# Performance work log

Measured on AMD Instinct MI355X. Metric: run time of the kernel, lower is better.

The kernel has to match this reference:

```python
import jax, jax.numpy as jnp
import numpy as np

N = 50000      # total nodes in batched graph
E = 800000     # total edges (avg degree 16)
B = 512        # number of graphs in batch
F_IN = 74      # input node feature size
H = 64         # hidden size per layer
OUT = 64       # output_feats
EPS = 1e-5     # BatchNorm eps


def setup_inputs() -> dict:
    key = jax.random.key(0)
    ks = jax.random.split(key, 32)
    d = {}
    d['feats'] = jax.random.normal(ks[0], (N, F_IN), dtype=jnp.float32)
    d['src'] = jax.random.randint(ks[1], (E,), 0, N)
    d['dst'] = jax.random.randint(ks[2], (E,), 0, N)
    d['graph_ids'] = jnp.sort(jax.random.randint(ks[3], (N,), 0, B))
    dims = [F_IN, H, H, H]
    i = 4
    for l in range(3):
        din, dout = dims[l], dims[l + 1]
        d[f'W{l}'] = jax.random.normal(ks[i], (din, dout), jnp.float32) / np.sqrt(din).astype(np.float32); i += 1
        d[f'b{l}'] = jnp.zeros((dout,), jnp.float32)
        d[f'rW{l}'] = jax.random.normal(ks[i], (din, dout), jnp.float32) / np.sqrt(din).astype(np.float32); i += 1
        d[f'rb{l}'] = jnp.zeros((dout,), jnp.float32)
        d[f'g{l}'] = jnp.ones((dout,), jnp.float32)    # BN gamma
        d[f'be{l}'] = jnp.zeros((dout,), jnp.float32)  # BN beta
    d['aw_W'] = jax.random.normal(ks[i], (H, 1), jnp.float32) / np.sqrt(H).astype(np.float32); i += 1
    d['aw_b'] = jnp.zeros((1,), jnp.float32)
    d['out_W'] = jax.random.normal(ks[i], (2 * H, OUT), jnp.float32) / np.sqrt(2 * H).astype(np.float32); i += 1
    d['out_b'] = jnp.zeros((OUT,), jnp.float32)
    return d


def _gcn_layer(x, src, dst, W, b, rW, rb, g, be):
    # GraphConv, norm='none': out = sum-aggregate(X W) + b, then relu
    xw = x @ W                                                    # [N, dout]
    agg = jax.ops.segment_sum(xw[src], dst, num_segments=N) + b   # gather/scatter over edges
    h = jax.nn.relu(agg)
    # residual: relu(Linear(x))
    h = h + jax.nn.relu(x @ rW + rb)
    # dropout p=0 -> identity
    # BatchNorm1d (training-mode batch statistics, biased variance)
    mean = jnp.mean(h, axis=0)
    var = jnp.var(h, axis=0)
    return (h - mean) * jax.lax.rsqrt(var + EPS) * g + be


def reference(feats, src, dst, graph_ids,
              W0, b0, rW0, rb0, g0, be0,
              W1, b1, rW1, rb1, g1, be1,
              W2, b2, rW2, rb2, g2, be2,
              aw_W, aw_b, out_W, out_b):
    h = feats
    h = _gcn_layer(h, src, dst, W0, b0, rW0, rb0, g0, be0)
    h = _gcn_layer(h, src, dst, W1, b1, rW1, rb1, g1, be1)
    h = _gcn_layer(h, src, dst, W2, b2, rW2, rb2, g2, be2)
    # WeightedSumAndMax readout
    w = jax.nn.sigmoid(h @ aw_W + aw_b)                               # [N, 1]
    h_sum = jax.ops.segment_sum(h * w, graph_ids, num_segments=B)     # [B, H]
    h_max = jax.ops.segment_max(h, graph_ids, num_segments=B)         # [B, H]
    h_max = jnp.where(jnp.isfinite(h_max), h_max, 0.0)                # empty graphs -> 0 (dgl max_nodes)
    h_g = jnp.concatenate([h_sum, h_max], axis=1)                     # [B, 2H]
    return h_g @ out_W + out_b                                        # [B, OUT]
```

## Files before the change

kernel.cpp:

```cpp
#include <hip/hip_runtime.h>
#include <hip/hip_bf16.h>
#include <math.h>

#define NN 50000
#define NE 800000
#define NB 512
#define FIN 74
#define HD 64
#define BN_EPS 1e-5f

#define CHUNK 32
#define ELLW 32
#define NBLK ((NN + CHUNK - 1) / CHUNK)
#define NBUCK2 NBLK
#define EB2 128
#define EPB (NE / EB2)
#define OCAP 512


__global__ void init_kernel(float* __restrict__ stats012,
                            unsigned long long* __restrict__ xw_zrow,
                            const float* __restrict__ W0, const float* __restrict__ rW0,
                            float2* __restrict__ Wpk0) {
    int i = blockIdx.x * 256 + threadIdx.x;
    if (i < 384) stats012[i] = 0.f;
    if (i < 16) xw_zrow[i] = 0ull;
    if (i < FIN * HD) Wpk0[i] = make_float2(W0[i], rW0[i]);
}

__global__ __launch_bounds__(256) void hist2_kernel(const int* __restrict__ dst,
                                                    int* __restrict__ H) {
    __shared__ int lh[NBUCK2];
    int b = blockIdx.x, tid = threadIdx.x;
    for (int i = tid; i < NBUCK2; i += 256) lh[i] = 0;
    __syncthreads();
    int e0 = b * EPB;
    for (int i = tid; i < EPB; i += 256) atomicAdd(&lh[dst[e0 + i] >> 5], 1);
    __syncthreads();
    for (int i = tid; i < NBUCK2; i += 256) H[b * NBUCK2 + i] = lh[i];
}

__global__ __launch_bounds__(128) void scanA2_kernel(int* __restrict__ H, int* __restrict__ T) {
    __shared__ int l[128];
    int k = blockIdx.x, tid = threadIdx.x;
    int v = H[tid * NBUCK2 + k];
    l[tid] = v;
    __syncthreads();
    for (int off = 1; off < 128; off <<= 1) {
        int t = (tid >= off) ? l[tid - off] : 0;
        __syncthreads();
        l[tid] += t;
        __syncthreads();
    }
    H[tid * NBUCK2 + k] = l[tid] - v;
    if (tid == 127) T[k] = l[127];
}

__global__ __launch_bounds__(256) void scanB2_kernel(const int* __restrict__ T,
                                                     int* __restrict__ bbase) {
    __shared__ int l[256];
    __shared__ int carry;
    int tid = threadIdx.x;
    if (tid == 0) carry = 0;
    __syncthreads();
    for (int c0 = 0; c0 < NBUCK2; c0 += 256) {
        int v = (c0 + tid < NBUCK2) ? T[c0 + tid] : 0;
        l[tid] = v;
        __syncthreads();
        for (int off = 1; off < 256; off <<= 1) {
            int t = (tid >= off) ? l[tid - off] : 0;
            __syncthreads();
            l[tid] += t;
            __syncthreads();
        }
        if (c0 + tid < NBUCK2) bbase[c0 + tid] = l[tid] - v + carry;
        __syncthreads();
        if (tid == 0) carry += l[255];
        __syncthreads();
    }
    if (tid == 0) bbase[NBUCK2] = carry;
}

__global__ __launch_bounds__(256) void addC_kernel(int* __restrict__ H,
                                                   const int* __restrict__ bbase) {
    int b = blockIdx.x;
    for (int k = threadIdx.x; k < NBUCK2; k += 256) H[b * NBUCK2 + k] += bbase[k];
}

__global__ __launch_bounds__(256) void scatter2_kernel(const int* __restrict__ src,
                                                       const int* __restrict__ dst,
                                                       const int* __restrict__ H,
                                                       unsigned* __restrict__ pairs) {
    __shared__ int cur[NBUCK2];
    int b = blockIdx.x, tid = threadIdx.x;
    for (int i = tid; i < NBUCK2; i += 256) cur[i] = H[b * NBUCK2 + i];
    __syncthreads();
    int e0 = b * EPB;
    for (int i = tid; i < EPB; i += 256) {
        int d = dst[e0 + i];
        int s = src[e0 + i];
        int pos = atomicAdd(&cur[d >> 5], 1);
        pairs[pos] = (unsigned)s | ((unsigned)(d & 31) << 17);
    }
}


template <int K>
__global__ __launch_bounds__(256) void gemm_dual_kernel(
    const float* __restrict__ x, const float2* __restrict__ Wpk,
    const float* __restrict__ rb, __hip_bfloat16* __restrict__ xw,
    __hip_bfloat16* __restrict__ res, int n) {
    __shared__ float2 sW[K * HD];
    __shared__ float srb[64];
    for (int i = threadIdx.x; i < K * HD; i += 256) sW[i] = Wpk[i];
    if (threadIdx.x < 64) srb[threadIdx.x] = rb[threadIdx.x];
    __syncthreads();
    int wl = threadIdx.x >> 6, lane = threadIdx.x & 63;
    for (int r0 = (blockIdx.x * 4 + wl) * 8; r0 < n; r0 += gridDim.x * 32) {
        float a1[8], a2[8];
#pragma unroll
        for (int r = 0; r < 8; ++r) { a1[r] = 0.f; a2[r] = 0.f; }
#pragma unroll
        for (int c0 = 0; c0 < K; c0 += 64) {
            const int cl = (K - c0 < 64) ? (K - c0) : 64;
            float xv[8];
#pragma unroll
            for (int r = 0; r < 8; ++r) {
                int row = r0 + r;
                xv[r] = (lane < cl && row < n) ? x[(size_t)row * K + c0 + lane] : 0.f;
            }
            for (int j = 0; j < cl; ++j) {
                float2 w = sW[(c0 + j) * HD + lane];
#pragma unroll
                for (int r = 0; r < 8; ++r) {
                    float xb = __uint_as_float(
                        __builtin_amdgcn_readlane(__float_as_uint(xv[r]), j));
                    a1[r] = fmaf(xb, w.x, a1[r]);
                    a2[r] = fmaf(xb, w.y, a2[r]);
                }
            }
        }
#pragma unroll
        for (int r = 0; r < 8; ++r) {
            int row = r0 + r;
            if (row < n) {
                xw[(size_t)row * HD + lane] = __float2bfloat16(a1[r]);
                res[(size_t)row * HD + lane] = __float2bfloat16(fmaxf(a2[r] + srb[lane], 0.f));
            }
        }
    }
}

__global__ void fold_kernel(const float* __restrict__ stats, const float* __restrict__ g,
                            const float* __restrict__ be, const float* __restrict__ W,
                            const float* __restrict__ rW, const float* __restrict__ rb,
                            float2* __restrict__ Wpk, float* __restrict__ shiftW,
                            float* __restrict__ rbp) {
    __shared__ float sc[64], sh[64];
    int t = threadIdx.x;
    if (t < 64) {
        float mean = stats[t] / (float)NN;
        float var = stats[64 + t] / (float)NN - mean * mean;
        float scale = g[t] * rsqrtf(var + BN_EPS);
        sc[t] = scale;
        sh[t] = be[t] - mean * scale;
    }
    __syncthreads();
    for (int i = t; i < 64 * 64; i += 256) {
        int k = i >> 6;
        Wpk[i] = make_float2(sc[k] * W[i], sc[k] * rW[i]);
    }
    if (t < 64) {
        float sw = 0.f, srw = 0.f;
        for (int k = 0; k < 64; ++k) {
            sw = fmaf(sh[k], W[k * 64 + t], sw);
            srw = fmaf(sh[k], rW[k * 64 + t], srw);
        }
        shiftW[t] = sw;
        rbp[t] = rb[t] + srw;
    }
}

__device__ __forceinline__ float bf_lo(unsigned int p) { return __uint_as_float(p << 16); }
__device__ __forceinline__ float bf_hi(unsigned int p) { return __uint_as_float(p & 0xffff0000u); }

#define GATHER16(BASE)                                             \
    {                                                              \
        unsigned long long d[16];                                  \
        _Pragma("unroll") for (int j = 0; j < 16; ++j) {           \
            int idx = sIdx[rloc][(BASE) + j];                      \
            unsigned off = (unsigned)idx * 16u + (unsigned)c8;     \
            d[j] = XWu[off];                                       \
        }                                                          \
        _Pragma("unroll") for (int j = 0; j < 16; ++j) {           \
            unsigned lo = (unsigned)d[j], hi = (unsigned)(d[j] >> 32); \
            a0 += bf_lo(lo); a1 += bf_hi(lo);                      \
            a2 += bf_lo(hi); a3 += bf_hi(hi);                      \
        }                                                          \
    }

__global__ __launch_bounds__(256, 4) void fused_agg_kernel(
    const __hip_bfloat16* __restrict__ xw, const __hip_bfloat16* __restrict__ res,
    const float* __restrict__ b, const float* __restrict__ shiftW,
    const int* __restrict__ bbase, const unsigned* __restrict__ pairs,
    float* __restrict__ hout, float* __restrict__ stats, int n) {
    __shared__ int sIdx[CHUNK][ELLW + 1];
    __shared__ int sLen[CHUNK];
    __shared__ unsigned oflow[OCAP];
    __shared__ int ocnt;
    __shared__ int sBB[2];
    __shared__ float sbb[128];
    __shared__ float lsr[4][16][8];

    int tid = threadIdx.x;
    int r0 = blockIdx.x * CHUNK;

    for (int i = tid; i < CHUNK * (ELLW + 1); i += 256) ((int*)sIdx)[i] = NN;
    if (tid < CHUNK) sLen[tid] = 0;
    if (tid == 0) ocnt = 0;
    if (tid < 2) sBB[tid] = bbase[blockIdx.x + tid];
    if (tid >= 128 && tid < 256) {
        int j = tid - 128;
        sbb[j] = (j < 64) ? b[j] : (shiftW ? shiftW[j - 64] : 0.f);
    }
    __syncthreads();
    int beg = sBB[0], end = sBB[1];
    for (int i = beg + tid; i < end; i += 256) {
        unsigned v = pairs[i];
        int rloc = (int)(v >> 17);
        int rk = atomicAdd(&sLen[rloc], 1);
        if (rk < ELLW) {
            sIdx[rloc][rk] = (int)(v & 0x1FFFFu);
        } else {
            int o = atomicAdd(&ocnt, 1);
            if (o < OCAP) oflow[o] = v;
        }
    }
    __syncthreads();
    int noflow = (ocnt < OCAP) ? ocnt : OCAP;

    const unsigned long long* XWu = (const unsigned long long*)xw;
    const unsigned long long* REu = (const unsigned long long*)res;
    int wl = tid >> 6, lane = tid & 63;
    int q = lane >> 4, c8 = lane & 15;
    float sb0 = sbb[4 * c8], sb1 = sbb[4 * c8 + 1], sb2 = sbb[4 * c8 + 2], sb3 = sbb[4 * c8 + 3];
    float sw0 = sbb[64 + 4 * c8], sw1 = sbb[64 + 4 * c8 + 1];
    float sw2 = sbb[64 + 4 * c8 + 2], sw3 = sbb[64 + 4 * c8 + 3];
    float s0 = 0.f, s1 = 0.f, s2 = 0.f, s3 = 0.f;
    float q0 = 0.f, q1 = 0.f, q2 = 0.f, q3 = 0.f;

#pragma unroll
    for (int p = 0; p < 2; ++p) {
        int rbase = wl * 8 + p * 4;
        int rloc = rbase + q;
        int grow = r0 + rloc;
        int growc = (grow < n) ? grow : (n - 1);
        int l0 = sLen[rbase], l1 = sLen[rbase + 1], l2 = sLen[rbase + 2], l3 = sLen[rbase + 3];
        int m01 = (l0 > l1) ? l0 : l1, m23 = (l2 > l3) ? l2 : l3;
        int kmax = (m01 > m23) ? m01 : m23;
        int mylen = sLen[rloc];
        unsigned long long rqw = REu[(unsigned)growc * 16u + (unsigned)c8];
        float a0 = 0.f, a1 = 0.f, a2 = 0.f, a3 = 0.f;
        GATHER16(0)
        if (kmax > 16) GATHER16(16)
        if (kmax > ELLW) {
            for (int o = 0; o < noflow; ++o) {
                unsigned v = oflow[o];
                if ((int)(v >> 17) == rloc) {
                    unsigned off = (v & 0x1FFFFu) * 16u + (unsigned)c8;
                    unsigned long long u = XWu[off];
                    unsigned lo = (unsigned)u, hi = (unsigned)(u >> 32);
                    a0 += bf_lo(lo); a1 += bf_hi(lo);
                    a2 += bf_lo(hi); a3 += bf_hi(hi);
                }
            }
        }
        unsigned rlo = (unsigned)rqw, rhi = (unsigned)(rqw >> 32);
        float dg = (float)mylen;
        float h0 = fmaxf(a0 + fmaf(dg, sw0, sb0), 0.f) + bf_lo(rlo);
        float h1 = fmaxf(a1 + fmaf(dg, sw1, sb1), 0.f) + bf_hi(rlo);
        float h2 = fmaxf(a2 + fmaf(dg, sw2, sb2), 0.f) + bf_lo(rhi);
        float h3 = fmaxf(a3 + fmaf(dg, sw3, sb3), 0.f) + bf_hi(rhi);
        if (grow < n) {
            *(float4*)&hout[(unsigned)grow * 64u + 4u * c8] = make_float4(h0, h1, h2, h3);
            s0 += h0; s1 += h1; s2 += h2; s3 += h3;
            q0 += h0 * h0; q1 += h1 * h1; q2 += h2 * h2; q3 += h3 * h3;
        }
    }

    s0 += __shfl_xor(s0, 16, 64); s0 += __shfl_xor(s0, 32, 64);
    s1 += __shfl_xor(s1, 16, 64); s1 += __shfl_xor(s1, 32, 64);
    s2 += __shfl_xor(s2, 16, 64); s2 += __shfl_xor(s2, 32, 64);
    s3 += __shfl_xor(s3, 16, 64); s3 += __shfl_xor(s3, 32, 64);
    q0 += __shfl_xor(q0, 16, 64); q0 += __shfl_xor(q0, 32, 64);
    q1 += __shfl_xor(q1, 16, 64); q1 += __shfl_xor(q1, 32, 64);
    q2 += __shfl_xor(q2, 16, 64); q2 += __shfl_xor(q2, 32, 64);
    q3 += __shfl_xor(q3, 16, 64); q3 += __shfl_xor(q3, 32, 64);
    if (q == 0) {
        lsr[wl][c8][0] = s0; lsr[wl][c8][1] = s1; lsr[wl][c8][2] = s2; lsr[wl][c8][3] = s3;
        lsr[wl][c8][4] = q0; lsr[wl][c8][5] = q1; lsr[wl][c8][6] = q2; lsr[wl][c8][7] = q3;
    }
    __syncthreads();
    if (tid < 64) {
        int c8i = tid >> 2, comp = tid & 3;
        float ssum = lsr[0][c8i][comp] + lsr[1][c8i][comp] + lsr[2][c8i][comp] + lsr[3][c8i][comp];
        float qsum = lsr[0][c8i][4 + comp] + lsr[1][c8i][4 + comp] + lsr[2][c8i][4 + comp] +
                     lsr[3][c8i][4 + comp];
        atomicAdd(&stats[tid], ssum);
        atomicAdd(&stats[64 + tid], qsum);
    }
}


__global__ void readout_init_kernel(float* __restrict__ hsum, unsigned int* __restrict__ hmax,
                                    const float* __restrict__ stats, const float* __restrict__ g,
                                    const float* __restrict__ be, float* __restrict__ ss) {
    int idx = blockIdx.x * 256 + threadIdx.x;
    if (idx < NB * HD) {
        hsum[idx] = 0.f;
        hmax[idx] = 0x007FFFFFu;
    }
    if (blockIdx.x == 0 && threadIdx.x < 64) {
        int c = threadIdx.x;
        float mean = stats[c] / (float)NN;
        float var = stats[64 + c] / (float)NN - mean * mean;
        float scale = g[c] * rsqrtf(var + BN_EPS);
        ss[c] = scale;
        ss[64 + c] = be[c] - mean * scale;
    }
}

#define RNODES 16

__device__ __forceinline__ void ro_flush(float* hsum, unsigned int* hmax, int g, int c,
                                         float accS, float accM) {
    atomicAdd(&hsum[g * HD + c], accS);
    unsigned int bits = __float_as_uint(accM);
    unsigned int enc = (bits & 0x80000000u) ? ~bits : (bits | 0x80000000u);
    atomicMax(&hmax[g * HD + c], enc);
}

__global__ __launch_bounds__(256) void readout_kernel(
    const float* __restrict__ h, const int* __restrict__ gid, const float* __restrict__ ss,
    const float* __restrict__ awW, const float* __restrict__ awb, float* __restrict__ hsum,
    unsigned int* __restrict__ hmax, int n) {
    int wid = blockIdx.x * 4 + (threadIdx.x >> 6);
    int c = threadIdx.x & 63;
    int r0 = wid * RNODES;
    if (r0 >= n) return;
    int r1 = r0 + RNODES;
    if (r1 > n) r1 = n;
    float aw = awW[c], ab = awb[0];
    float sA = ss[c], sB = ss[64 + c];
    int cur = gid[r0];
    float accS = 0.f, accM = -__builtin_inff();
    for (int r = r0; r < r1; ++r) {
        int g = gid[r];
        if (g != cur) {
            ro_flush(hsum, hmax, cur, c, accS, accM);
            accS = 0.f;
            accM = -__builtin_inff();
            cur = g;
        }
        float v = fmaf(h[(size_t)r * HD + c], sA, sB);
        float p = v * aw;
        for (int off = 32; off; off >>= 1) p += __shfl_xor(p, off, 64);
        float w = 1.f / (1.f + expf(-(p + ab)));
        accS = fmaf(v, w, accS);
        accM = fmaxf(accM, v);
    }
    ro_flush(hsum, hmax, cur, c, accS, accM);
}

__global__ void final_kernel(const float* __restrict__ hsum, const unsigned int* __restrict__ hmax,
                             const float* __restrict__ outW, const float* __restrict__ outb,
                             float* __restrict__ out) {
    __shared__ float sW[128 * 64];
    for (int i = threadIdx.x; i < 128 * 64; i += 256) sW[i] = outW[i];
    __syncthreads();
    int idx = blockIdx.x * 256 + threadIdx.x;
    if (idx >= NB * HD) return;
    int bi = idx >> 6, o = idx & 63;
    float acc = outb[o];
#pragma unroll 4
    for (int k = 0; k < 64; ++k) acc = fmaf(hsum[bi * 64 + k], sW[k * 64 + o], acc);
#pragma unroll 4
    for (int k = 0; k < 64; ++k) {
        unsigned int e = hmax[bi * 64 + k];
        float m;
        if (e == 0x007FFFFFu) {
            m = 0.f;
        } else {
            m = (e & 0x80000000u) ? __uint_as_float(e ^ 0x80000000u) : __uint_as_float(~e);
        }
        acc = fmaf(m, sW[(64 + k) * 64 + o], acc);
    }
    out[idx] = acc;
}


extern "C" void kernel_launch(void* const* d_in, const int* in_sizes, int n_in,
                              void* d_out, int out_size, void* d_ws, size_t ws_size,
                              hipStream_t stream) {
    const float* feats = (const float*)d_in[0];
    const int* src = (const int*)d_in[1];
    const int* dst = (const int*)d_in[2];
    const int* gid = (const int*)d_in[3];
    const float* W[3];
    const float* b[3];
    const float* rW[3];
    const float* rb[3];
    const float* g[3];
    const float* be[3];
    for (int l = 0; l < 3; ++l) {
        W[l] = (const float*)d_in[4 + 6 * l + 0];
        b[l] = (const float*)d_in[4 + 6 * l + 1];
        rW[l] = (const float*)d_in[4 + 6 * l + 2];
        rb[l] = (const float*)d_in[4 + 6 * l + 3];
        g[l] = (const float*)d_in[4 + 6 * l + 4];
        be[l] = (const float*)d_in[4 + 6 * l + 5];
    }
    const float* awW = (const float*)d_in[22];
    const float* awb = (const float*)d_in[23];
    const float* outW = (const float*)d_in[24];
    const float* outb = (const float*)d_in[25];
    float* out = (float*)d_out;

    __hip_bfloat16* XW = (__hip_bfloat16*)d_ws;
    __hip_bfloat16* RES = XW + (size_t)(NN + 1) * HD;
    float* P1 = (float*)(RES + (size_t)NN * HD);
    float* stats = P1 + (size_t)NN * HD;
    float* ss2 = stats + 384;
    float2* WPK = (float2*)(ss2 + 128);
    float* shW = (float*)(WPK + FIN * HD);
    float* rbp = shW + 64;
    float* hsum = rbp + 64;
    unsigned int* hmax = (unsigned int*)(hsum + (size_t)NB * HD);
    unsigned* pairs = (unsigned*)(hmax + (size_t)NB * HD);
    int* H = (int*)(pairs + (size_t)NE);
    int* T = H + (size_t)EB2 * NBUCK2;
    int* bbase = T + NBUCK2;

    float* stats0 = stats;
    float* stats1 = stats + 128;
    float* stats2 = stats + 256;

    const int GEMMBLK = 1280;
    const int ROBLK = (NN + RNODES * 4 - 1) / (RNODES * 4);

    init_kernel<<<(FIN * HD + 255) / 256, 256, 0, stream>>>(
        stats, (unsigned long long*)(XW + (size_t)NN * HD), W[0], rW[0], WPK);
    hist2_kernel<<<EB2, 256, 0, stream>>>(dst, H);
    scanA2_kernel<<<NBUCK2, 128, 0, stream>>>(H, T);
    scanB2_kernel<<<1, 256, 0, stream>>>(T, bbase);
    addC_kernel<<<EB2, 256, 0, stream>>>(H, bbase);
    scatter2_kernel<<<EB2, 256, 0, stream>>>(src, dst, H, pairs);

    gemm_dual_kernel<FIN><<<GEMMBLK, 256, 0, stream>>>(feats, WPK, rb[0], XW, RES, NN);
    fused_agg_kernel<<<NBLK, 256, 0, stream>>>(XW, RES, b[0], (const float*)nullptr, bbase,
                                               pairs, P1, stats0, NN);

    fold_kernel<<<1, 256, 0, stream>>>(stats0, g[0], be[0], W[1], rW[1], rb[1], WPK, shW, rbp);
    gemm_dual_kernel<HD><<<GEMMBLK, 256, 0, stream>>>(P1, WPK, rbp, XW, RES, NN);
    fused_agg_kernel<<<NBLK, 256, 0, stream>>>(XW, RES, b[1], shW, bbase, pairs, P1, stats1, NN);

    fold_kernel<<<1, 256, 0, stream>>>(stats1, g[1], be[1], W[2], rW[2], rb[2], WPK, shW, rbp);
    gemm_dual_kernel<HD><<<GEMMBLK, 256, 0, stream>>>(P1, WPK, rbp, XW, RES, NN);
    fused_agg_kernel<<<NBLK, 256, 0, stream>>>(XW, RES, b[2], shW, bbase, pairs, P1, stats2, NN);

    readout_init_kernel<<<(NB * HD + 255) / 256, 256, 0, stream>>>(hsum, hmax, stats2, g[2], be[2], ss2);
    readout_kernel<<<ROBLK, 256, 0, stream>>>(P1, gid, ss2, awW, awb, hsum, hmax, NN);
    final_kernel<<<(NB * HD + 255) / 256, 256, 0, stream>>>(hsum, hmax, outW, outb, out);
}
```

Before: 323.0 us.

## Fold init and addC kernels, make per-wave ELL build in aggregation

Moves the init work into the first block of the histogram kernel and folds the bucket-base add into the scatter kernel, removing two kernel launches. In the fused aggregation kernel each wavefront now builds its own 8-row ELL index lists and overflow buffer. Each wave scans the whole block's edge range but keeps only the edges for its own rows, so the block-wide __syncthreads barriers go away. Bias and shift are read straight from global memory, and launch bounds are raised to 6 blocks per CU. The cost is that every wave reads the block's edge pairs four times, and a smaller overflow capacity is kept per wave.

After: 323.2 us. Within noise of the previous version (+0.1%).

```diff
diff --git a/kernel.cpp b/kernel.cpp
--- a/kernel.cpp
+++ b/kernel.cpp
@@ -15,27 +15,27 @@
 #define NBUCK2 NBLK
 #define EB2 128
 #define EPB (NE / EB2)
-#define OCAP 512
-
-
-__global__ void init_kernel(float* __restrict__ stats012,
-                            unsigned long long* __restrict__ xw_zrow,
-                            const float* __restrict__ W0, const float* __restrict__ rW0,
-                            float2* __restrict__ Wpk0) {
-    int i = blockIdx.x * 256 + threadIdx.x;
-    if (i < 384) stats012[i] = 0.f;
-    if (i < 16) xw_zrow[i] = 0ull;
-    if (i < FIN * HD) Wpk0[i] = make_float2(W0[i], rW0[i]);
-}
+#define OCAPW 96
+
 
 __global__ __launch_bounds__(256) void hist2_kernel(const int* __restrict__ dst,
-                                                    int* __restrict__ H) {
+                                                    int* __restrict__ H,
+                                                    float* __restrict__ stats012,
+                                                    unsigned long long* __restrict__ xw_zrow,
+                                                    const float* __restrict__ W0,
+                                                    const float* __restrict__ rW0,
+                                                    float2* __restrict__ Wpk0) {
     __shared__ int lh[NBUCK2];
     int b = blockIdx.x, tid = threadIdx.x;
     for (int i = tid; i < NBUCK2; i += 256) lh[i] = 0;
     __syncthreads();
     int e0 = b * EPB;
     for (int i = tid; i < EPB; i += 256) atomicAdd(&lh[dst[e0 + i] >> 5], 1);
+    if (b == 0) {
+        for (int i = tid; i < 384; i += 256) stats012[i] = 0.f;
+        if (tid < 16) xw_zrow[tid] = 0ull;
+        for (int i = tid; i < FIN * HD; i += 256) Wpk0[i] = make_float2(W0[i], rW0[i]);
+    }
     __syncthreads();
     for (int i = tid; i < NBUCK2; i += 256) H[b * NBUCK2 + i] = lh[i];
 }
@@ -81,19 +81,14 @@
     if (tid == 0) bbase[NBUCK2] = carry;
 }
 
-__global__ __launch_bounds__(256) void addC_kernel(int* __restrict__ H,
-                                                   const int* __restrict__ bbase) {
-    int b = blockIdx.x;
-    for (int k = threadIdx.x; k < NBUCK2; k += 256) H[b * NBUCK2 + k] += bbase[k];
-}
-
 __global__ __launch_bounds__(256) void scatter2_kernel(const int* __restrict__ src,
                                                        const int* __restrict__ dst,
                                                        const int* __restrict__ H,
+                                                       const int* __restrict__ bbase,
                                                        unsigned* __restrict__ pairs) {
     __shared__ int cur[NBUCK2];
     int b = blockIdx.x, tid = threadIdx.x;
-    for (int i = tid; i < NBUCK2; i += 256) cur[i] = H[b * NBUCK2 + i];
+    for (int i = tid; i < NBUCK2; i += 256) cur[i] = H[b * NBUCK2 + i] + bbase[i];
     __syncthreads();
     int e0 = b * EPB;
     for (int i = tid; i < EPB; i += 256) {
@@ -188,7 +183,7 @@
     {                                                              \
         unsigned long long d[16];                                  \
         _Pragma("unroll") for (int j = 0; j < 16; ++j) {           \
-            int idx = sIdx[rloc][(BASE) + j];                      \
+            int idx = myIdx[(BASE) + j];                           \
             unsigned off = (unsigned)idx * 16u + (unsigned)c8;     \
             d[j] = XWu[off];                                       \
         }                                                          \
@@ -199,74 +194,71 @@
         }                                                          \
     }
 
-__global__ __launch_bounds__(256, 4) void fused_agg_kernel(
+__global__ __launch_bounds__(256, 6) void fused_agg_kernel(
     const __hip_bfloat16* __restrict__ xw, const __hip_bfloat16* __restrict__ res,
     const float* __restrict__ b, const float* __restrict__ shiftW,
     const int* __restrict__ bbase, const unsigned* __restrict__ pairs,
     float* __restrict__ hout, float* __restrict__ stats, int n) {
-    __shared__ int sIdx[CHUNK][ELLW + 1];
-    __shared__ int sLen[CHUNK];
-    __shared__ unsigned oflow[OCAP];
-    __shared__ int ocnt;
-    __shared__ int sBB[2];
-    __shared__ float sbb[128];
+    __shared__ int sIdx[4][8][ELLW + 1];
+    __shared__ int sLen[4][8];
+    __shared__ unsigned oflow[4][OCAPW];
+    __shared__ int ocnt[4];
     __shared__ float lsr[4][16][8];
 
     int tid = threadIdx.x;
+    int wl = tid >> 6, lane = tid & 63;
     int r0 = blockIdx.x * CHUNK;
 
-    for (int i = tid; i < CHUNK * (ELLW + 1); i += 256) ((int*)sIdx)[i] = NN;
-    if (tid < CHUNK) sLen[tid] = 0;
-    if (tid == 0) ocnt = 0;
-    if (tid < 2) sBB[tid] = bbase[blockIdx.x + tid];
-    if (tid >= 128 && tid < 256) {
-        int j = tid - 128;
-        sbb[j] = (j < 64) ? b[j] : (shiftW ? shiftW[j - 64] : 0.f);
-    }
-    __syncthreads();
-    int beg = sBB[0], end = sBB[1];
-    for (int i = beg + tid; i < end; i += 256) {
+    for (int i = lane; i < 8 * (ELLW + 1); i += 64) ((int*)sIdx[wl])[i] = NN;
+    if (lane < 8) sLen[wl][lane] = 0;
+    if (lane == 0) ocnt[wl] = 0;
+
+    int beg = bbase[blockIdx.x], end = bbase[blockIdx.x + 1];
+    for (int i = beg + lane; i < end; i += 64) {
         unsigned v = pairs[i];
         int rloc = (int)(v >> 17);
-        int rk = atomicAdd(&sLen[rloc], 1);
-        if (rk < ELLW) {
-            sIdx[rloc][rk] = (int)(v & 0x1FFFFu);
-        } else {
-            int o = atomicAdd(&ocnt, 1);
-            if (o < OCAP) oflow[o] = v;
-        }
-    }
-    __syncthreads();
-    int noflow = (ocnt < OCAP) ? ocnt : OCAP;
+        if ((rloc >> 3) == wl) {
+            int r8 = rloc & 7;
+            int rk = atomicAdd(&sLen[wl][r8], 1);
+            if (rk < ELLW) {
+                sIdx[wl][r8][rk] = (int)(v & 0x1FFFFu);
+            } else {
+                int o = atomicAdd(&ocnt[wl], 1);
+                if (o < OCAPW) oflow[wl][o] = v;
+            }
+        }
+    }
+    int nof = ocnt[wl];
+    int noflow = (nof < OCAPW) ? nof : OCAPW;
 
     const unsigned long long* XWu = (const unsigned long long*)xw;
     const unsigned long long* REu = (const unsigned long long*)res;
-    int wl = tid >> 6, lane = tid & 63;
     int q = lane >> 4, c8 = lane & 15;
-    float sb0 = sbb[4 * c8], sb1 = sbb[4 * c8 + 1], sb2 = sbb[4 * c8 + 2], sb3 = sbb[4 * c8 + 3];
-    float sw0 = sbb[64 + 4 * c8], sw1 = sbb[64 + 4 * c8 + 1];
-    float sw2 = sbb[64 + 4 * c8 + 2], sw3 = sbb[64 + 4 * c8 + 3];
+    float4 bv = *(const float4*)&b[4 * c8];
+    float4 swv = shiftW ? *(const float4*)&shiftW[4 * c8] : make_float4(0.f, 0.f, 0.f, 0.f);
     float s0 = 0.f, s1 = 0.f, s2 = 0.f, s3 = 0.f;
     float q0 = 0.f, q1 = 0.f, q2 = 0.f, q3 = 0.f;
 
 #pragma unroll
     for (int p = 0; p < 2; ++p) {
-        int rbase = wl * 8 + p * 4;
-        int rloc = rbase + q;
-        int grow = r0 + rloc;
+        int r8 = p * 4 + q;
+        int grow = r0 + wl * 8 + r8;
         int growc = (grow < n) ? grow : (n - 1);
-        int l0 = sLen[rbase], l1 = sLen[rbase + 1], l2 = sLen[rbase + 2], l3 = sLen[rbase + 3];
+        int l0 = sLen[wl][p * 4], l1 = sLen[wl][p * 4 + 1];
+        int l2 = sLen[wl][p * 4 + 2], l3 = sLen[wl][p * 4 + 3];
         int m01 = (l0 > l1) ? l0 : l1, m23 = (l2 > l3) ? l2 : l3;
         int kmax = (m01 > m23) ? m01 : m23;
-        int mylen = sLen[rloc];
+        int mylen = sLen[wl][r8];
+        const int* myIdx = sIdx[wl][r8];
         unsigned long long rqw = REu[(unsigned)growc * 16u + (unsigned)c8];
         float a0 = 0.f, a1 = 0.f, a2 = 0.f, a3 = 0.f;
         GATHER16(0)
         if (kmax > 16) GATHER16(16)
         if (kmax > ELLW) {
+            int myrloc = wl * 8 + r8;
             for (int o = 0; o < noflow; ++o) {
-                unsigned v = oflow[o];
-                if ((int)(v >> 17) == rloc) {
+                unsigned v = oflow[wl][o];
+                if ((int)(v >> 17) == myrloc) {
                     unsigned off = (v & 0x1FFFFu) * 16u + (unsigned)c8;
                     unsigned long long u = XWu[off];
                     unsigned lo = (unsigned)u, hi = (unsigned)(u >> 32);
@@ -277,10 +269,10 @@
         }
         unsigned rlo = (unsigned)rqw, rhi = (unsigned)(rqw >> 32);
         float dg = (float)mylen;
-        float h0 = fmaxf(a0 + fmaf(dg, sw0, sb0), 0.f) + bf_lo(rlo);
-        float h1 = fmaxf(a1 + fmaf(dg, sw1, sb1), 0.f) + bf_hi(rlo);
-        float h2 = fmaxf(a2 + fmaf(dg, sw2, sb2), 0.f) + bf_lo(rhi);
-        float h3 = fmaxf(a3 + fmaf(dg, sw3, sb3), 0.f) + bf_hi(rhi);
+        float h0 = fmaxf(a0 + fmaf(dg, swv.x, bv.x), 0.f) + bf_lo(rlo);
+        float h1 = fmaxf(a1 + fmaf(dg, swv.y, bv.y), 0.f) + bf_hi(rlo);
+        float h2 = fmaxf(a2 + fmaf(dg, swv.z, bv.z), 0.f) + bf_lo(rhi);
+        float h3 = fmaxf(a3 + fmaf(dg, swv.w, bv.w), 0.f) + bf_hi(rhi);
         if (grow < n) {
             *(float4*)&hout[(unsigned)grow * 64u + 4u * c8] = make_float4(h0, h1, h2, h3);
             s0 += h0; s1 += h1; s2 += h2; s3 += h3;
@@ -448,13 +440,12 @@
     const int GEMMBLK = 1280;
     const int ROBLK = (NN + RNODES * 4 - 1) / (RNODES * 4);
 
-    init_kernel<<<(FIN * HD + 255) / 256, 256, 0, stream>>>(
-        stats, (unsigned long long*)(XW + (size_t)NN * HD), W[0], rW[0], WPK);
-    hist2_kernel<<<EB2, 256, 0, stream>>>(dst, H);
+    hist2_kernel<<<EB2, 256, 0, stream>>>(dst, H, stats,
+                                          (unsigned long long*)(XW + (size_t)NN * HD),
+                                          W[0], rW[0], WPK);
     scanA2_kernel<<<NBUCK2, 128, 0, stream>>>(H, T);
     scanB2_kernel<<<1, 256, 0, stream>>>(T, bbase);
-    addC_kernel<<<EB2, 256, 0, stream>>>(H, bbase);
-    scatter2_kernel<<<EB2, 256, 0, stream>>>(src, dst, H, pairs);
+    scatter2_kernel<<<EB2, 256, 0, stream>>>(src, dst, H, bbase, pairs);
 
     gemm_dual_kernel<FIN><<<GEMMBLK, 256, 0, stream>>>(feats, WPK, rb[0], XW, RES, NN);
     fused_agg_kernel<<<NBLK, 256, 0, stream>>>(XW, RES, b[0], (const float*)nullptr, bbase,
```
